# Performance work log

Measured on AMD Instinct MI355X. Metric: run time of the kernel, lower is better.

The kernel has to match this reference:

```python
import jax, jax.numpy as jnp
import numpy as np

EPS = 1e-6

def setup_inputs() -> dict:
    key = jax.random.key(0)
    kq, kk, kv = jax.random.split(key, 3)
    n, L, h, d = 4, 8192, 8, 64
    queries = jax.random.normal(kq, (n, L, h, d), dtype=jnp.float32)
    keys = jax.random.normal(kk, (n, L, h, d), dtype=jnp.float32)
    values = jax.random.normal(kv, (n, L, h, d), dtype=jnp.float32)
    return {"queries": queries, "keys": keys, "values": values}

def reference(queries, keys, values):
    d = queries.shape[-1]
    temp = d ** (-0.25)  # softmax_temp default e**-0.25
    # elu feature map: phi(x) = elu(x) + 1  (applied after temperature scaling)
    q = jax.nn.elu(queries * temp) + 1.0  # [n, l, h, d]
    k = jax.nn.elu(keys * temp) + 1.0     # [n, s, h, d]
    # associative kv state: [n, h, m, d]
    kv = jnp.einsum('nshd,nshm->nhmd', k, values)
    # normalizer z: [n, l, h]
    z = 1.0 / (jnp.einsum('nlhd,nhd->nlh', q, k.sum(axis=1)) + EPS)
    # output: [n, l, h, m]
    v = jnp.einsum('nlhd,nhmd,nlh->nlhm', q, kv, z)
    # module returns v.transpose(-3, -2) -> [n, h, l, m]
    return jnp.swapaxes(v, 1, 2)
```

## Files before the change

### kernel.cpp

```cpp
#include <hip/hip_runtime.h>
#include <hip/hip_bf16.h>

#define NN 4
#define LL 8192
#define HH 8
#define DD 64
#define NH 32
#define RS  (HH*DD)
#define KV_ELEMS 4160
#define CCH 128

typedef __attribute__((ext_vector_type(8))) short bf16x8;
typedef __attribute__((ext_vector_type(4))) float f32x4;

__device__ __forceinline__ float phi(float x) {
  float t = x * 0.35355339059327373f;
  return t > 0.f ? t + 1.f : __expf(t);
}
__device__ __forceinline__ short f2bf(float x) {
  __hip_bfloat16 h = __float2bfloat16(x);
  return (short)__builtin_bit_cast(unsigned short, h);
}
__device__ __forceinline__ float bf2f(short s) {
  __hip_bfloat16 h = __builtin_bit_cast(__hip_bfloat16, (unsigned short)s);
  return __bfloat162float(h);
}
__device__ __forceinline__ void split2(float x, short& hi, short& lo) {
  hi = f2bf(x);
  lo = f2bf(x - bf2f(hi));
}
#define MFMA16 __builtin_amdgcn_mfma_f32_16x16x32_bf16

__global__ __launch_bounds__(512, 2) void kv_partial_kernel(
    const float* __restrict__ K, const float* __restrict__ V,
    float* __restrict__ part, int sch)
{
  const int n = blockIdx.x / sch, chunk = blockIdx.x % sch;
  const int tid = threadIdx.x;
  const int h  = tid >> 6;
  const int t6 = tid & 63;
  const int d0 = ((t6 >> 3) & 7) * 8;
  const int m0 = (t6 & 7) * 8;
  const int hc = h * 64;
  const int sr = tid >> 6, sc = (tid & 63) * 8;
  const int rows_pb = LL / sch;
  const int nt = rows_pb / 8;

  const float* kbase = K + ((size_t)n * LL + (size_t)chunk * rows_pb) * RS;
  const float* vbase = V + ((size_t)n * LL + (size_t)chunk * rows_pb) * RS;

  __shared__ float kls[8][520];
  __shared__ float vls[8][520];

  float acc[8][8] = {};
  float ksacc[8] = {};
  f32x4 kr[2], vr[2];

  auto loada = [&](int T) {
    const float* kp_ = kbase + ((size_t)T * 8 + sr) * RS + sc;
    const float* vp_ = vbase + ((size_t)T * 8 + sr) * RS + sc;
    kr[0] = *(const f32x4*)(kp_);     kr[1] = *(const f32x4*)(kp_ + 4);
    vr[0] = *(const f32x4*)(vp_);     vr[1] = *(const f32x4*)(vp_ + 4);
  };

  loada(0);
  for (int t = 0; t < nt; ++t) {
    f32x4 kw0, kw1;
#pragma unroll
    for (int jj = 0; jj < 4; ++jj) {
      float f0 = phi(kr[0][jj]);
      float f1 = phi(kr[1][jj]);
      ksacc[jj]     += f0;
      ksacc[jj + 4] += f1;
      kw0[jj] = f0; kw1[jj] = f1;
    }
    *(f32x4*)&kls[sr][sc]     = kw0;
    *(f32x4*)&kls[sr][sc + 4] = kw1;
    *(f32x4*)&vls[sr][sc]     = vr[0];
    *(f32x4*)&vls[sr][sc + 4] = vr[1];
    __syncthreads();
    if (t + 1 < nt) loada(t + 1);

#pragma unroll 2
    for (int s = 0; s < 8; ++s) {
      const f32x4 k0 = *(const f32x4*)&kls[s][hc + d0];
      const f32x4 k1 = *(const f32x4*)&kls[s][hc + d0 + 4];
      const f32x4 v0 = *(const f32x4*)&vls[s][hc + m0];
      const f32x4 v1 = *(const f32x4*)&vls[s][hc + m0 + 4];
#pragma unroll
      for (int i = 0; i < 4; ++i)
#pragma unroll
        for (int j = 0; j < 4; ++j) {
          acc[i][j]         = fmaf(k0[i], v0[j], acc[i][j]);
          acc[i][j + 4]     = fmaf(k0[i], v1[j], acc[i][j + 4]);
          acc[i + 4][j]     = fmaf(k1[i], v0[j], acc[i + 4][j]);
          acc[i + 4][j + 4] = fmaf(k1[i], v1[j], acc[i + 4][j + 4]);
        }
    }
    __syncthreads();
  }

  float* po = part + ((size_t)blockIdx.x * 8 + h) * KV_ELEMS;
#pragma unroll
  for (int i = 0; i < 8; ++i) {
    f32x4 o0 = {acc[i][0], acc[i][1], acc[i][2], acc[i][3]};
    f32x4 o1 = {acc[i][4], acc[i][5], acc[i][6], acc[i][7]};
    *(f32x4*)&po[(d0 + i) * 64 + m0]     = o0;
    *(f32x4*)&po[(d0 + i) * 64 + m0 + 4] = o1;
  }

#pragma unroll
  for (int j = 0; j < 8; ++j) vls[sr][sc + j] = ksacc[j];
  __syncthreads();
  {
    float s = 0.f;
#pragma unroll
    for (int r = 0; r < 8; ++r) s += vls[r][tid];
    part[((size_t)blockIdx.x * 8 + (tid >> 6)) * KV_ELEMS + 4096 + (tid & 63)] = s;
  }
}

__global__ __launch_bounds__(256) void kv_reduce_kernel(
    const float* __restrict__ part, short* __restrict__ kvh,
    short* __restrict__ kvl, float* __restrict__ ksum, int np)
{
  const int nh = blockIdx.x / 17;
  const int e  = (blockIdx.x % 17) * 256 + threadIdx.x;
  if (e >= KV_ELEMS) return;
  const int n = nh >> 3, hh = nh & 7;
  const float* pp = part + ((size_t)(n * np) * 8 + hh) * KV_ELEMS + e;
  float s = 0.f;
  for (int i = 0; i < np; ++i) s += pp[(size_t)i * 8 * KV_ELEMS];
  if (e < 4096) {
    const int d = e >> 6, m = e & 63;
    short hi, lo; split2(s, hi, lo);
    kvh[(size_t)nh * 4096 + m * 64 + d] = hi;
    kvl[(size_t)nh * 4096 + m * 64 + d] = lo;
  } else {
    ksum[(size_t)nh * 64 + (e - 4096)] = s;
  }
}

__global__ __launch_bounds__(512, 2) void attn_out_kernel(
    const float* __restrict__ Q, const short* __restrict__ kvh,
    const short* __restrict__ kvl, const float* __restrict__ ksumg,
    float* __restrict__ out)
{
  const int n = blockIdx.x / CCH, chunk = blockIdx.x % CCH;
  const int tid = threadIdx.x;
  const int w = tid >> 6, lane = tid & 63;
  const int q = lane >> 4, p = lane & 15;
  const int nh = n * 8 + w;
  const int rows_pb = LL / CCH;
  const int nt = rows_pb / 16;
  const int l_base = chunk * rows_pb;
  const int sr = tid >> 5, sc = (tid & 31) * 16;

  const float* qbase = Q + (size_t)n * LL * RS;

  __shared__ short qh[16][520];
  __shared__ short ql[16][520];

  bf16x8 bh[4][2], bl[4][2];
#pragma unroll
  for (int mt = 0; mt < 4; ++mt)
#pragma unroll
    for (int kst = 0; kst < 2; ++kst) {
      const size_t off = (size_t)nh * 4096 + (size_t)(mt * 16 + p) * 64 + kst * 32 + q * 8;
      bh[mt][kst] = *(const bf16x8*)(kvh + off);
      bl[mt][kst] = *(const bf16x8*)(kvl + off);
    }
  float ksr[2][8];
#pragma unroll
  for (int kst = 0; kst < 2; ++kst) {
    const float* kp = ksumg + (size_t)nh * 64 + kst * 32 + q * 8;
    f32x4 a = *(const f32x4*)(kp), b = *(const f32x4*)(kp + 4);
    ksr[kst][0]=a[0]; ksr[kst][1]=a[1]; ksr[kst][2]=a[2]; ksr[kst][3]=a[3];
    ksr[kst][4]=b[0]; ksr[kst][5]=b[1]; ksr[kst][6]=b[2]; ksr[kst][7]=b[3];
  }

  f32x4 qa[4], qb[4];
  auto loadq = [&](f32x4* R, int T) {
    const float* qp_ = qbase + (size_t)(l_base + T * 16 + sr) * RS + sc;
    R[0] = *(const f32x4*)(qp_);      R[1] = *(const f32x4*)(qp_ + 4);
    R[2] = *(const f32x4*)(qp_ + 8);  R[3] = *(const f32x4*)(qp_ + 12);
  };

  auto cbody = [&](const f32x4* R, int T) {
    bf16x8 hv0, hv1, lv0, lv1;
#pragma unroll
    for (int r = 0; r < 2; ++r)
#pragma unroll
      for (int jj = 0; jj < 4; ++jj) {
        float f = phi(R[r][jj]);
        short hs, ls; split2(f, hs, ls);
        hv0[r * 4 + jj] = hs; lv0[r * 4 + jj] = ls;
      }
#pragma unroll
    for (int r = 0; r < 2; ++r)
#pragma unroll
      for (int jj = 0; jj < 4; ++jj) {
        float f = phi(R[r + 2][jj]);
        short hs, ls; split2(f, hs, ls);
        hv1[r * 4 + jj] = hs; lv1[r * 4 + jj] = ls;
      }
    *(bf16x8*)&qh[sr][sc]     = hv0;  *(bf16x8*)&qh[sr][sc + 8] = hv1;
    *(bf16x8*)&ql[sr][sc]     = lv0;  *(bf16x8*)&ql[sr][sc + 8] = lv1;
    __syncthreads();

    f32x4 acc[4] = {};
    float zp = 0.f;
    bf16x8 ah[2], al[2];
#pragma unroll
    for (int kst = 0; kst < 2; ++kst) {
      const int cc = w * 64 + kst * 32 + q * 8;
      ah[kst] = *(const bf16x8*)&qh[p][cc];
      al[kst] = *(const bf16x8*)&ql[p][cc];
#pragma unroll
      for (int j = 0; j < 8; ++j)
        zp += (bf2f(ah[kst][j]) + bf2f(al[kst][j])) * ksr[kst][j];
    }
#pragma unroll
    for (int kst = 0; kst < 2; ++kst)
#pragma unroll
      for (int mt = 0; mt < 4; ++mt) {
        acc[mt] = MFMA16(ah[kst], bh[mt][kst], acc[mt], 0, 0, 0);
        acc[mt] = MFMA16(ah[kst], bl[mt][kst], acc[mt], 0, 0, 0);
        acc[mt] = MFMA16(al[kst], bh[mt][kst], acc[mt], 0, 0, 0);
      }
    zp += __shfl_xor(zp, 16, 64);
    zp += __shfl_xor(zp, 32, 64);
    const float z = 1.0f / (zp + 1e-6f);
    float zr[4];
#pragma unroll
    for (int r = 0; r < 4; ++r) zr[r] = __shfl(z, q * 4 + r, 64);

    const int l0 = l_base + T * 16;
#pragma unroll
    for (int mt = 0; mt < 4; ++mt)
#pragma unroll
      for (int r = 0; r < 4; ++r)
        out[((size_t)nh * LL + l0 + q * 4 + r) * DD + mt * 16 + p] = acc[mt][r] * zr[r];
    __syncthreads();
  };

  loadq(qa, 0);
  for (int t = 0; t < nt; t += 2) {
    loadq(qb, t + 1);
    cbody(qa, t);
    if (t + 2 < nt) loadq(qa, t + 2);
    cbody(qb, t + 1);
  }
}

extern "C" void kernel_launch(void* const* d_in, const int* in_sizes, int n_in,
                              void* d_out, int out_size, void* d_ws, size_t ws_size,
                              hipStream_t stream)
{
  const float* Q = (const float*)d_in[0];
  const float* K = (const float*)d_in[1];
  const float* V = (const float*)d_in[2];
  float* out = (float*)d_out;

  int sch = 128;
  while (sch > 4) {
    size_t need = (size_t)NN * sch * 8 * KV_ELEMS * 4
                + (size_t)NH * 4096 * 2 * 2
                + (size_t)NH * 64 * 4;
    if (need <= ws_size) break;
    sch >>= 1;
  }
  float* part = (float*)d_ws;
  short* kvh  = (short*)((char*)d_ws + (size_t)NN * sch * 8 * KV_ELEMS * 4);
  short* kvl  = kvh + (size_t)NH * 4096;
  float* ksum = (float*)(kvl + (size_t)NH * 4096);

  hipLaunchKernelGGL(kv_partial_kernel, dim3(NN * sch), dim3(512), 0, stream,
                     K, V, part, sch);
  hipLaunchKernelGGL(kv_reduce_kernel, dim3(NH * 17), dim3(256), 0, stream,
                     part, kvh, kvl, ksum, sch);
  hipLaunchKernelGGL(attn_out_kernel, dim3(NN * CCH), dim3(512), 0, stream,
                     Q, kvh, kvl, ksum, out);
}
```

Before: 266.6 us.

## Double-buffer LDS tiles of 16 rows in kv_partial and halve chunk count

```diff
diff --git a/kernel.cpp b/kernel.cpp
--- a/kernel.cpp
+++ b/kernel.cpp
@@ -9,6 +9,7 @@
 #define RS  (HH*DD)
 #define KV_ELEMS 4160
 #define CCH 128
+#define TILE 16
 
 typedef __attribute__((ext_vector_type(8))) short bf16x8;
 typedef __attribute__((ext_vector_type(4))) float f32x4;
@@ -31,7 +32,7 @@
 }
 #define MFMA16 __builtin_amdgcn_mfma_f32_16x16x32_bf16
 
-__global__ __launch_bounds__(512, 2) void kv_partial_kernel(
+__global__ __launch_bounds__(512, 1) void kv_partial_kernel(
     const float* __restrict__ K, const float* __restrict__ V,
     float* __restrict__ part, int sch)
 {
@@ -42,51 +43,57 @@
   const int d0 = ((t6 >> 3) & 7) * 8;
   const int m0 = (t6 & 7) * 8;
   const int hc = h * 64;
-  const int sr = tid >> 6, sc = (tid & 63) * 8;
+  const int sr = tid >> 5;
+  const int sc = (tid & 31) * 16;
   const int rows_pb = LL / sch;
-  const int nt = rows_pb / 8;
+  const int nt = rows_pb / TILE;
 
   const float* kbase = K + ((size_t)n * LL + (size_t)chunk * rows_pb) * RS;
   const float* vbase = V + ((size_t)n * LL + (size_t)chunk * rows_pb) * RS;
 
-  __shared__ float kls[8][520];
-  __shared__ float vls[8][520];
+  __shared__ float lds[2][2][TILE][520];
 
   float acc[8][8] = {};
-  float ksacc[8] = {};
-  f32x4 kr[2], vr[2];
-
-  auto loada = [&](int T) {
-    const float* kp_ = kbase + ((size_t)T * 8 + sr) * RS + sc;
-    const float* vp_ = vbase + ((size_t)T * 8 + sr) * RS + sc;
-    kr[0] = *(const f32x4*)(kp_);     kr[1] = *(const f32x4*)(kp_ + 4);
-    vr[0] = *(const f32x4*)(vp_);     vr[1] = *(const f32x4*)(vp_ + 4);
-  };
-
-  loada(0);
+  float ksacc[16] = {};
+  f32x4 kr[4], vr[4];
+
+  auto loadregs = [&](int T) {
+    const float* kp = kbase + ((size_t)T * TILE + sr) * RS + sc;
+    const float* vp = vbase + ((size_t)T * TILE + sr) * RS + sc;
+#pragma unroll
+    for (int i = 0; i < 4; ++i) {
+      kr[i] = *(const f32x4*)(kp + 4 * i);
+      vr[i] = *(const f32x4*)(vp + 4 * i);
+    }
+  };
+  auto stage = [&](int b) {
+#pragma unroll
+    for (int i = 0; i < 4; ++i) {
+      f32x4 kw;
+#pragma unroll
+      for (int j = 0; j < 4; ++j) {
+        float f = phi(kr[i][j]);
+        ksacc[4 * i + j] += f;
+        kw[j] = f;
+      }
+      *(f32x4*)&lds[b][0][sr][sc + 4 * i] = kw;
+      *(f32x4*)&lds[b][1][sr][sc + 4 * i] = vr[i];
+    }
+  };
+
+  loadregs(0);
+  stage(0);
+  __syncthreads();
+
   for (int t = 0; t < nt; ++t) {
-    f32x4 kw0, kw1;
-#pragma unroll
-    for (int jj = 0; jj < 4; ++jj) {
-      float f0 = phi(kr[0][jj]);
-      float f1 = phi(kr[1][jj]);
-      ksacc[jj]     += f0;
-      ksacc[jj + 4] += f1;
-      kw0[jj] = f0; kw1[jj] = f1;
-    }
-    *(f32x4*)&kls[sr][sc]     = kw0;
-    *(f32x4*)&kls[sr][sc + 4] = kw1;
-    *(f32x4*)&vls[sr][sc]     = vr[0];
-    *(f32x4*)&vls[sr][sc + 4] = vr[1];
-    __syncthreads();
-    if (t + 1 < nt) loada(t + 1);
-
+    const int cur = t & 1;
+    if (t + 1 < nt) loadregs(t + 1);
 #pragma unroll 2
-    for (int s = 0; s < 8; ++s) {
-      const f32x4 k0 = *(const f32x4*)&kls[s][hc + d0];
-      const f32x4 k1 = *(const f32x4*)&kls[s][hc + d0 + 4];
-      const f32x4 v0 = *(const f32x4*)&vls[s][hc + m0];
-      const f32x4 v1 = *(const f32x4*)&vls[s][hc + m0 + 4];
+    for (int s = 0; s < TILE; ++s) {
+      const f32x4 k0 = *(const f32x4*)&lds[cur][0][s][hc + d0];
+      const f32x4 k1 = *(const f32x4*)&lds[cur][0][s][hc + d0 + 4];
+      const f32x4 v0 = *(const f32x4*)&lds[cur][1][s][hc + m0];
+      const f32x4 v1 = *(const f32x4*)&lds[cur][1][s][hc + m0 + 4];
 #pragma unroll
       for (int i = 0; i < 4; ++i)
 #pragma unroll
@@ -97,6 +104,7 @@
           acc[i + 4][j + 4] = fmaf(k1[i], v1[j], acc[i + 4][j + 4]);
         }
     }
+    if (t + 1 < nt) stage(cur ^ 1);
     __syncthreads();
   }
 
@@ -110,13 +118,16 @@
   }
 
 #pragma unroll
-  for (int j = 0; j < 8; ++j) vls[sr][sc + j] = ksacc[j];
+  for (int i = 0; i < 4; ++i) {
+    f32x4 kw = {ksacc[4 * i], ksacc[4 * i + 1], ksacc[4 * i + 2], ksacc[4 * i + 3]};
+    *(f32x4*)&lds[0][0][sr][sc + 4 * i] = kw;
+  }
   __syncthreads();
   {
-    float s = 0.f;
-#pragma unroll
-    for (int r = 0; r < 8; ++r) s += vls[r][tid];
-    part[((size_t)blockIdx.x * 8 + (tid >> 6)) * KV_ELEMS + 4096 + (tid & 63)] = s;
+    float ssum = 0.f;
+#pragma unroll
+    for (int r = 0; r < TILE; ++r) ssum += lds[0][0][r][tid];
+    part[((size_t)blockIdx.x * 8 + (tid >> 6)) * KV_ELEMS + 4096 + (tid & 63)] = ssum;
   }
 }
 
@@ -262,7 +273,7 @@
   const float* V = (const float*)d_in[2];
   float* out = (float*)d_out;
 
-  int sch = 128;
+  int sch = 64;
   while (sch > 4) {
     size_t need = (size_t)NN * sch * 8 * KV_ELEMS * 4
                 + (size_t)NH * 4096 * 2 * 2
```

After: 247.1 us. 7.3% less time.
